# Kernel optimization log

Measured on AMD Instinct MI355X. Metric: run time of the kernel, lower is better.

## Reference

```python
import jax, jax.numpy as jnp
import numpy as np

B, S, D_MODEL, N_HEADS = 4, 2048, 1024, 16
HEAD_DIM = D_MODEL // N_HEADS


def setup_inputs() -> dict:
    key = jax.random.key(0)
    k_x, k_wqkv, k_bqkv, k_wout, k_bout = jax.random.split(key, 5)
    x = jax.random.normal(k_x, (B, S, D_MODEL), dtype=jnp.float32)
    # causal mask: True = masked (matches masked_fill semantics)
    mask = jnp.triu(jnp.ones((S, S), dtype=bool), k=1)[None, None, :, :]
    sc = 1.0 / np.sqrt(D_MODEL)
    w_qkv = jax.random.normal(k_wqkv, (3 * D_MODEL, D_MODEL), dtype=jnp.float32) * sc
    b_qkv = jax.random.normal(k_bqkv, (3 * D_MODEL,), dtype=jnp.float32) * 0.02
    w_out = jax.random.normal(k_wout, (D_MODEL, D_MODEL), dtype=jnp.float32) * sc
    b_out = jax.random.normal(k_bout, (D_MODEL,), dtype=jnp.float32) * 0.02
    return {"x": x, "mask": mask, "w_qkv": w_qkv, "b_qkv": b_qkv,
            "w_out": w_out, "b_out": b_out}


def reference(x, mask, w_qkv, b_qkv, w_out, b_out):
    b, s, d = x.shape
    qkv = x @ w_qkv.T + b_qkv                      # [B,S,3*D]
    qkv = qkv.reshape(b, s, 3, N_HEADS, HEAD_DIM)
    q = qkv[:, :, 0].transpose(0, 2, 1, 3)         # [B,H,S,Dh]
    k = qkv[:, :, 1].transpose(0, 2, 1, 3)
    v = qkv[:, :, 2].transpose(0, 2, 1, 3)
    scores = jnp.einsum('bhqd,bhkd->bhqk', q, k) / np.sqrt(HEAD_DIM)
    scores = jnp.where(mask, -jnp.inf, scores)
    attn = jax.nn.softmax(scores, axis=-1)         # dropout p=0.0 -> identity
    ctx = jnp.einsum('bhqk,bhkd->bhqd', attn, v)   # [B,H,S,Dh]
    ctx = ctx.transpose(0, 2, 1, 3).reshape(b, s, d)
    return ctx @ w_out.T + b_out
```

## Files before the change

kernel.cpp:

```cpp
#include <hip/hip_runtime.h>
#include <stdint.h>

typedef __attribute__((ext_vector_type(8))) short bf16x8;
typedef __attribute__((ext_vector_type(4))) float f32x4;
typedef unsigned short u16;

#define NUM_B 4
#define SEQ   2048
#define DM    1024
#define NH    16
#define DH    64
#define M_TOT (NUM_B * SEQ)

__device__ __forceinline__ float bf2f(u16 u) {
    union { unsigned int i; float f; } c; c.i = ((unsigned int)u) << 16; return c.f;
}
__device__ __forceinline__ u16 f2bf(float f) {
    union { float f; unsigned int i; } c; c.f = f;
    unsigned int u = c.i;
    return (u16)((u + 0x7FFFu + ((u >> 16) & 1u)) >> 16);
}
__device__ __forceinline__ unsigned int pack2(float a, float b) {
    return (unsigned int)f2bf(a) | ((unsigned int)f2bf(b) << 16);
}

__device__ __forceinline__ u16 f2bf_hw(float a) {
    unsigned int r;
    asm("v_cvt_pk_bf16_f32 %0, %1, %2" : "=v"(r) : "v"(a), "v"(0.0f));
    return (u16)r;
}

#if __has_builtin(__builtin_amdgcn_exp2f)
#define EXP2F __builtin_amdgcn_exp2f
#else
#define EXP2F exp2f
#endif

#define GLOAD_LDS16(g, l)                                                     \
    __builtin_amdgcn_global_load_lds(                                         \
        (const __attribute__((address_space(1))) void*)(g),                   \
        (__attribute__((address_space(3))) void*)(l), 16, 0, 0)

__global__ void detect_dtype(const u16* __restrict__ x, int* __restrict__ flag) {
    __shared__ int cnt;
    if (threadIdx.x == 0) cnt = 0;
    __syncthreads();
    int local = 0;
    for (int i = threadIdx.x; i < 4096; i += 256) {
        const u16 v = x[i];
        const int e = (v >> 7) & 0xFF;
        if (v == 0 || (e >= 110 && e <= 145)) local++;
    }
    atomicAdd(&cnt, local);
    __syncthreads();
    if (threadIdx.x == 0) *flag = (cnt >= 3686) ? 0 : 1;
}

__global__ void convert_bf16(const void* __restrict__ in, u16* __restrict__ out,
                             long n, const int* __restrict__ flag)
{
    const long i0 = ((long)blockIdx.x * 256 + threadIdx.x) * 8;
    const long stride = (long)gridDim.x * 256 * 8;
    if (*flag) {
        const float* f = (const float*)in;
        for (long i = i0; i < n; i += stride) {
            float4 a = *(const float4*)(f + i);
            float4 b = *(const float4*)(f + i + 4);
            uint4 o;
            o.x = pack2(a.x, a.y); o.y = pack2(a.z, a.w);
            o.z = pack2(b.x, b.y); o.w = pack2(b.z, b.w);
            *(uint4*)(out + i) = o;
        }
    } else {
        const uint4* s = (const uint4*)in;
        for (long i = i0; i < n; i += stride)
            *(uint4*)(out + i) = s[i >> 3];
    }
}

template <int MODE, int N_TOT>
__global__ __launch_bounds__(256) void gemm_bt(
    const u16* __restrict__ A, const u16* __restrict__ Bm,
    const u16* __restrict__ bias,
    void* __restrict__ out0v, u16* __restrict__ out1, u16* __restrict__ out2,
    const int* __restrict__ outf32, long out_off)
{
    __shared__ __align__(16) u16 As[128 * 32];
    __shared__ __align__(16) u16 Bs[128 * 32];
    const int K = 1024;

    const int tid  = threadIdx.x;
    const int wave = tid >> 6;
    const int lane = tid & 63;
    const int l15  = lane & 15;
    const int quad = lane >> 4;

    const int m0 = blockIdx.y * 128;
    const int n0 = blockIdx.x * 128;
    const int wm = (wave >> 1) * 64;
    const int wn = (wave & 1) * 64;

    const int srow = lane >> 2;
    const int soff = (lane & 3) * 8;

    f32x4 acc[4][4];
#pragma unroll
    for (int i = 0; i < 4; ++i)
#pragma unroll
        for (int j = 0; j < 4; ++j)
            acc[i][j] = (f32x4){0.f, 0.f, 0.f, 0.f};

    for (int k0 = 0; k0 < K; k0 += 32) {
#pragma unroll
        for (int r = 0; r < 2; ++r) {
            const int chunk = wave * 2 + r;
            const int row   = chunk * 16 + srow;
            GLOAD_LDS16(&A[(size_t)(m0 + row) * K + k0 + soff], &As[chunk * 512]);
            GLOAD_LDS16(&Bm[(size_t)(n0 + row) * K + k0 + soff], &Bs[chunk * 512]);
        }
        __syncthreads();

        bf16x8 af[4], bfv[4];
#pragma unroll
        for (int i = 0; i < 4; ++i)
            af[i] = *(const bf16x8*)(&As[(wm + i * 16 + l15) * 32 + quad * 8]);
#pragma unroll
        for (int j = 0; j < 4; ++j)
            bfv[j] = *(const bf16x8*)(&Bs[(wn + j * 16 + l15) * 32 + quad * 8]);

#pragma unroll
        for (int i = 0; i < 4; ++i)
#pragma unroll
            for (int j = 0; j < 4; ++j)
                acc[i][j] = __builtin_amdgcn_mfma_f32_16x16x32_bf16(
                    af[i], bfv[j], acc[i][j], 0, 0, 0);
        __syncthreads();
    }

    const int of32 = outf32 ? *outf32 : 0;
#pragma unroll
    for (int j = 0; j < 4; ++j) {
        const int n  = n0 + wn + j * 16 + l15;
        const float bv = bf2f(bias[n]);
#pragma unroll
        for (int i = 0; i < 4; ++i) {
#pragma unroll
            for (int reg = 0; reg < 4; ++reg) {
                const int m = m0 + wm + i * 16 + quad * 4 + reg;
                const float v = acc[i][j][reg] + bv;
                if (MODE == 0) {
                    const int sel = n >> 10;
                    const int h   = (n >> 6) & 15;
                    const int dh  = n & 63;
                    const int b   = m >> 11;
                    const int s   = m & 2047;
                    if (sel == 2) {
                        out2[((size_t)((b * NH + h) * DH + dh)) * SEQ + s] = f2bf(v);
                    } else {
                        u16* dst = (sel == 0) ? (u16*)out0v : out1;
                        dst[((size_t)((b * NH + h) * SEQ + s)) * DH + dh] = f2bf(v);
                    }
                } else {
                    if (of32)
                        ((float*)out0v)[out_off + (size_t)m * N_TOT + n] = v;
                    else
                        ((u16*)out0v)[out_off + (size_t)m * N_TOT + n] = f2bf(v);
                }
            }
        }
    }
}

__global__ __launch_bounds__(256) void attn_fwd(
    const u16* __restrict__ Qb, const u16* __restrict__ Kb,
    const u16* __restrict__ Vt, u16* __restrict__ ctx)
{
    __shared__ __align__(16) u16 Ks[2][2048];
    __shared__ __align__(16) u16 Vs[2][2048];
    __shared__ __align__(16) short Pbuf[4][2][16 * 40];

    const int tid  = threadIdx.x;
    const int wave = tid >> 6;
    const int lane = tid & 63;
    const int l15  = lane & 15;
    const int quad = lane >> 4;

    const int bh = blockIdx.x;
    const int yb = blockIdx.y;
    const int qrowA = (wave < 2) ? (yb * 64 + wave * 32)
                                 : (1984 - yb * 64 + (wave - 2) * 32);
    const int mkt   = qrowA >> 5;
    const int ktend = 63 - 2 * yb;

    const size_t base  = (size_t)bh * SEQ * DH;
    const size_t baseT = (size_t)bh * DH * SEQ;
    const float sc_l2e = 0.18033688011112042f;

    bf16x8 qf[2][2];
#pragma unroll
    for (int f = 0; f < 2; ++f)
#pragma unroll
        for (int c = 0; c < 2; ++c)
            qf[f][c] = *(const bf16x8*)(&Qb[base + (size_t)(qrowA + f * 16 + l15) * DH + c * 32 + quad * 8]);

    f32x4 acc[2][4];
#pragma unroll
    for (int f = 0; f < 2; ++f)
#pragma unroll
        for (int j = 0; j < 4; ++j) acc[f][j] = (f32x4){0.f, 0.f, 0.f, 0.f};
    float lsum[2][4] = {{0.f, 0.f, 0.f, 0.f}, {0.f, 0.f, 0.f, 0.f}};

    const int k_r = (wave & 1) * 16 + l15;
    const int k_c = ((wave >> 1) * 4 + quad) * 8;
    const int v_dh = wave * 16 + l15;
    const int v_k  = quad * 8;

    {
        GLOAD_LDS16(&Kb[base + (size_t)k_r * DH + k_c], &Ks[0][wave * 512]);
        GLOAD_LDS16(&Vt[baseT + (size_t)v_dh * SEQ + v_k], &Vs[0][wave * 512]);
    }

    for (int kt = 0; kt <= ktend; ++kt) {
        const int cur = kt & 1;
        __syncthreads();

        if (kt + 1 <= ktend) {
            const int nk0 = (kt + 1) * 32;
            GLOAD_LDS16(&Kb[base + (size_t)(nk0 + k_r) * DH + k_c],
                        &Ks[1 - cur][wave * 512]);
            GLOAD_LDS16(&Vt[baseT + (size_t)v_dh * SEQ + nk0 + v_k],
                        &Vs[1 - cur][wave * 512]);
        }

        if (kt <= mkt) {
            bf16x8 kf[2][2], vfr[4];
#pragma unroll
            for (int half = 0; half < 2; ++half)
#pragma unroll
                for (int c = 0; c < 2; ++c)
                    kf[half][c] = *(const bf16x8*)(&Ks[cur][(c * 2 + half) * 512 + lane * 8]);
#pragma unroll
            for (int j = 0; j < 4; ++j)
                vfr[j] = *(const bf16x8*)(&Vs[cur][j * 512 + lane * 8]);

            const int diag = (kt == mkt);
#pragma unroll
            for (int f = 0; f < 2; ++f) {
                f32x4 sc0 = (f32x4){0.f, 0.f, 0.f, 0.f};
                f32x4 sc1 = (f32x4){0.f, 0.f, 0.f, 0.f};
                sc0 = __builtin_amdgcn_mfma_f32_16x16x32_bf16(qf[f][0], kf[0][0], sc0, 0, 0, 0);
                sc0 = __builtin_amdgcn_mfma_f32_16x16x32_bf16(qf[f][1], kf[0][1], sc0, 0, 0, 0);
                sc1 = __builtin_amdgcn_mfma_f32_16x16x32_bf16(qf[f][0], kf[1][0], sc1, 0, 0, 0);
                sc1 = __builtin_amdgcn_mfma_f32_16x16x32_bf16(qf[f][1], kf[1][1], sc1, 0, 0, 0);

                float pa[4], pb[4];
                if (diag) {
#pragma unroll
                    for (int r = 0; r < 4; ++r) {
                        const int rr = quad * 4 + r;
                        if (f == 0) {
                            pa[r] = (l15 <= rr) ? EXP2F(sc0[r] * sc_l2e) : 0.f;
                            pb[r] = 0.f;
                        } else {
                            pa[r] = EXP2F(sc0[r] * sc_l2e);
                            pb[r] = (l15 <= rr) ? EXP2F(sc1[r] * sc_l2e) : 0.f;
                        }
                    }
                } else {
#pragma unroll
                    for (int r = 0; r < 4; ++r) {
                        pa[r] = EXP2F(sc0[r] * sc_l2e);
                        pb[r] = EXP2F(sc1[r] * sc_l2e);
                    }
                }
#pragma unroll
                for (int r = 0; r < 4; ++r)
                    lsum[f][r] += pa[r] + pb[r];

                short* pw = Pbuf[wave][f];
                asm volatile("" ::: "memory");
#pragma unroll
                for (int r = 0; r < 4; ++r) {
                    const int row = quad * 4 + r;
                    pw[row * 40 + l15]      = (short)f2bf_hw(pa[r]);
                    pw[row * 40 + 16 + l15] = (short)f2bf_hw(pb[r]);
                }
                asm volatile("" ::: "memory");
                const bf16x8 pf = *(const bf16x8*)(&pw[l15 * 40 + quad * 8]);

#pragma unroll
                for (int j = 0; j < 4; ++j)
                    acc[f][j] = __builtin_amdgcn_mfma_f32_16x16x32_bf16(pf, vfr[j], acc[f][j], 0, 0, 0);
            }
        }
    }

#pragma unroll
    for (int off = 1; off <= 8; off <<= 1)
#pragma unroll
        for (int f = 0; f < 2; ++f)
#pragma unroll
            for (int r = 0; r < 4; ++r)
                lsum[f][r] += __shfl_xor(lsum[f][r], off);

    const int b = bh >> 4;
    const int h = bh & 15;
#pragma unroll
    for (int f = 0; f < 2; ++f) {
#pragma unroll
        for (int r = 0; r < 4; ++r) {
            const float invL = 1.0f / lsum[f][r];
            const int qrow = qrowA + f * 16 + quad * 4 + r;
            const size_t rowaddr = ((size_t)(b * SEQ + qrow)) * DM + h * DH;
#pragma unroll
            for (int j = 0; j < 4; ++j)
                ctx[rowaddr + j * 16 + l15] = f2bf_hw(acc[f][j][r] * invL);
        }
    }
}

extern "C" void kernel_launch(void* const* d_in, const int* in_sizes, int n_in,
                              void* d_out, int out_size, void* d_ws, size_t ws_size,
                              hipStream_t stream)
{
    auto find = [&](long want, int fb) -> const void* {
        for (int i = 0; i < n_in; ++i)
            if ((long)in_sizes[i] == want) return d_in[i];
        if (fb >= n_in) fb = n_in - 1;
        return d_in[fb];
    };
    const void* x     = find(8388608, 0);
    const void* w_qkv = find(3145728, 2);
    const void* b_qkv = find(3072,    3);
    const void* w_out = find(1048576, 4);
    const void* b_out = find(1024,    5);

    char* ws   = (char*)d_ws;
    int*  flag = (int*)ws;
    char* p    = ws + 256;

    u16* xbf    = (u16*)p;                 p += (size_t)8388608 * 2;
    u16* wqkvbf = (u16*)p;                 p += (size_t)3145728 * 2;
    u16* bqkvbf = (u16*)p;                 p += 8192;
    u16* woutbf = (u16*)p;                 p += (size_t)1048576 * 2;
    u16* boutbf = (u16*)p;                 p += 8192;

    const size_t tensor_bytes = (size_t)M_TOT * DM * sizeof(u16);
    const size_t chunk_bytes  = tensor_bytes / NUM_B;
    const size_t conv_end     = (size_t)(p - ws);

    detect_dtype<<<1, 256, 0, stream>>>((const u16*)x, flag);
    auto cgrid = [](long n) { long g = (n / 8 + 255) / 256; return (int)(g > 2048 ? 2048 : g); };
    convert_bf16<<<cgrid(8388608), 256, 0, stream>>>(x,     xbf,    8388608, flag);
    convert_bf16<<<cgrid(3145728), 256, 0, stream>>>(w_qkv, wqkvbf, 3145728, flag);
    convert_bf16<<<cgrid(3072),    256, 0, stream>>>(b_qkv, bqkvbf, 3072,    flag);
    convert_bf16<<<cgrid(1048576), 256, 0, stream>>>(w_out, woutbf, 1048576, flag);
    convert_bf16<<<cgrid(1024),    256, 0, stream>>>(b_out, boutbf, 1024,    flag);

    if (ws_size >= conv_end + 4 * tensor_bytes) {
        u16* Qb  = (u16*)(ws + conv_end);
        u16* Kb  = (u16*)(ws + conv_end + tensor_bytes);
        u16* Vb  = (u16*)(ws + conv_end + 2 * tensor_bytes);
        u16* ctx = (u16*)(ws + conv_end + 3 * tensor_bytes);

        gemm_bt<0, 3072><<<dim3(24, 64), 256, 0, stream>>>(
            xbf, wqkvbf, bqkvbf, Qb, Kb, Vb, nullptr, 0);
        attn_fwd<<<dim3(NUM_B * NH, SEQ / 128), 256, 0, stream>>>(Qb, Kb, Vb, ctx);
        gemm_bt<1, 1024><<<dim3(8, 64), 256, 0, stream>>>(
            ctx, woutbf, boutbf, d_out, nullptr, nullptr, flag, 0);
    } else {
        u16* Qb  = (u16*)(ws + conv_end);
        u16* Kb  = (u16*)(ws + conv_end + chunk_bytes);
        u16* Vb  = (u16*)(ws + conv_end + 2 * chunk_bytes);
        u16* ctx = (u16*)(ws + conv_end + 3 * chunk_bytes);
        for (int b = 0; b < NUM_B; ++b) {
            const long eoff = (long)b * SEQ * DM;
            gemm_bt<0, 3072><<<dim3(24, 16), 256, 0, stream>>>(
                xbf + eoff, wqkvbf, bqkvbf, Qb, Kb, Vb, nullptr, 0);
            attn_fwd<<<dim3(NH, SEQ / 128), 256, 0, stream>>>(Qb, Kb, Vb, ctx);
            gemm_bt<1, 1024><<<dim3(8, 16), 256, 0, stream>>>(
                ctx, woutbf, boutbf, d_out, nullptr, nullptr, flag, eoff);
        }
    }
}
```

Measured before the change: 351.5 us.

## Load K/V fragments directly from global memory, drop LDS staging and block syncs

New measurement: 366.0 us. 4.1% more time.

```diff
diff --git a/kernel.cpp b/kernel.cpp
--- a/kernel.cpp
+++ b/kernel.cpp
@@ -175,8 +175,6 @@
     const u16* __restrict__ Qb, const u16* __restrict__ Kb,
     const u16* __restrict__ Vt, u16* __restrict__ ctx)
 {
-    __shared__ __align__(16) u16 Ks[2][2048];
-    __shared__ __align__(16) u16 Vs[2][2048];
     __shared__ __align__(16) short Pbuf[4][2][16 * 40];
 
     const int tid  = threadIdx.x;
@@ -190,7 +188,6 @@
     const int qrowA = (wave < 2) ? (yb * 64 + wave * 32)
                                  : (1984 - yb * 64 + (wave - 2) * 32);
     const int mkt   = qrowA >> 5;
-    const int ktend = 63 - 2 * yb;
 
     const size_t base  = (size_t)bh * SEQ * DH;
     const size_t baseT = (size_t)bh * DH * SEQ;
@@ -210,88 +207,69 @@
         for (int j = 0; j < 4; ++j) acc[f][j] = (f32x4){0.f, 0.f, 0.f, 0.f};
     float lsum[2][4] = {{0.f, 0.f, 0.f, 0.f}, {0.f, 0.f, 0.f, 0.f}};
 
-    const int k_r = (wave & 1) * 16 + l15;
-    const int k_c = ((wave >> 1) * 4 + quad) * 8;
-    const int v_dh = wave * 16 + l15;
-    const int v_k  = quad * 8;
-
-    {
-        GLOAD_LDS16(&Kb[base + (size_t)k_r * DH + k_c], &Ks[0][wave * 512]);
-        GLOAD_LDS16(&Vt[baseT + (size_t)v_dh * SEQ + v_k], &Vs[0][wave * 512]);
-    }
-
-    for (int kt = 0; kt <= ktend; ++kt) {
-        const int cur = kt & 1;
-        __syncthreads();
-
-        if (kt + 1 <= ktend) {
-            const int nk0 = (kt + 1) * 32;
-            GLOAD_LDS16(&Kb[base + (size_t)(nk0 + k_r) * DH + k_c],
-                        &Ks[1 - cur][wave * 512]);
-            GLOAD_LDS16(&Vt[baseT + (size_t)v_dh * SEQ + nk0 + v_k],
-                        &Vs[1 - cur][wave * 512]);
-        }
-
-        if (kt <= mkt) {
-            bf16x8 kf[2][2], vfr[4];
-#pragma unroll
-            for (int half = 0; half < 2; ++half)
-#pragma unroll
-                for (int c = 0; c < 2; ++c)
-                    kf[half][c] = *(const bf16x8*)(&Ks[cur][(c * 2 + half) * 512 + lane * 8]);
-#pragma unroll
-            for (int j = 0; j < 4; ++j)
-                vfr[j] = *(const bf16x8*)(&Vs[cur][j * 512 + lane * 8]);
-
-            const int diag = (kt == mkt);
-#pragma unroll
-            for (int f = 0; f < 2; ++f) {
-                f32x4 sc0 = (f32x4){0.f, 0.f, 0.f, 0.f};
-                f32x4 sc1 = (f32x4){0.f, 0.f, 0.f, 0.f};
-                sc0 = __builtin_amdgcn_mfma_f32_16x16x32_bf16(qf[f][0], kf[0][0], sc0, 0, 0, 0);
-                sc0 = __builtin_amdgcn_mfma_f32_16x16x32_bf16(qf[f][1], kf[0][1], sc0, 0, 0, 0);
-                sc1 = __builtin_amdgcn_mfma_f32_16x16x32_bf16(qf[f][0], kf[1][0], sc1, 0, 0, 0);
-                sc1 = __builtin_amdgcn_mfma_f32_16x16x32_bf16(qf[f][1], kf[1][1], sc1, 0, 0, 0);
-
-                float pa[4], pb[4];
-                if (diag) {
-#pragma unroll
-                    for (int r = 0; r < 4; ++r) {
-                        const int rr = quad * 4 + r;
-                        if (f == 0) {
-                            pa[r] = (l15 <= rr) ? EXP2F(sc0[r] * sc_l2e) : 0.f;
-                            pb[r] = 0.f;
-                        } else {
-                            pa[r] = EXP2F(sc0[r] * sc_l2e);
-                            pb[r] = (l15 <= rr) ? EXP2F(sc1[r] * sc_l2e) : 0.f;
-                        }
-                    }
-                } else {
-#pragma unroll
-                    for (int r = 0; r < 4; ++r) {
+    for (int kt = 0; kt <= mkt; ++kt) {
+        const int k0 = kt * 32;
+
+        bf16x8 kf[2][2], vfr[4];
+#pragma unroll
+        for (int half = 0; half < 2; ++half)
+#pragma unroll
+            for (int c = 0; c < 2; ++c)
+                kf[half][c] = *(const bf16x8*)(
+                    &Kb[base + (size_t)(k0 + half * 16 + l15) * DH + c * 32 + quad * 8]);
+#pragma unroll
+        for (int j = 0; j < 4; ++j)
+            vfr[j] = *(const bf16x8*)(
+                &Vt[baseT + (size_t)(j * 16 + l15) * SEQ + k0 + quad * 8]);
+
+        const int diag = (kt == mkt);
+#pragma unroll
+        for (int f = 0; f < 2; ++f) {
+            f32x4 sc0 = (f32x4){0.f, 0.f, 0.f, 0.f};
+            f32x4 sc1 = (f32x4){0.f, 0.f, 0.f, 0.f};
+            sc0 = __builtin_amdgcn_mfma_f32_16x16x32_bf16(qf[f][0], kf[0][0], sc0, 0, 0, 0);
+            sc0 = __builtin_amdgcn_mfma_f32_16x16x32_bf16(qf[f][1], kf[0][1], sc0, 0, 0, 0);
+            sc1 = __builtin_amdgcn_mfma_f32_16x16x32_bf16(qf[f][0], kf[1][0], sc1, 0, 0, 0);
+            sc1 = __builtin_amdgcn_mfma_f32_16x16x32_bf16(qf[f][1], kf[1][1], sc1, 0, 0, 0);
+
+            float pa[4], pb[4];
+            if (diag) {
+#pragma unroll
+                for (int r = 0; r < 4; ++r) {
+                    const int rr = quad * 4 + r;
+                    if (f == 0) {
+                        pa[r] = (l15 <= rr) ? EXP2F(sc0[r] * sc_l2e) : 0.f;
+                        pb[r] = 0.f;
+                    } else {
                         pa[r] = EXP2F(sc0[r] * sc_l2e);
-                        pb[r] = EXP2F(sc1[r] * sc_l2e);
+                        pb[r] = (l15 <= rr) ? EXP2F(sc1[r] * sc_l2e) : 0.f;
                     }
                 }
-#pragma unroll
-                for (int r = 0; r < 4; ++r)
-                    lsum[f][r] += pa[r] + pb[r];
-
-                short* pw = Pbuf[wave][f];
-                asm volatile("" ::: "memory");
+            } else {
 #pragma unroll
                 for (int r = 0; r < 4; ++r) {
-                    const int row = quad * 4 + r;
-                    pw[row * 40 + l15]      = (short)f2bf_hw(pa[r]);
-                    pw[row * 40 + 16 + l15] = (short)f2bf_hw(pb[r]);
+                    pa[r] = EXP2F(sc0[r] * sc_l2e);
+                    pb[r] = EXP2F(sc1[r] * sc_l2e);
                 }
-                asm volatile("" ::: "memory");
-                const bf16x8 pf = *(const bf16x8*)(&pw[l15 * 40 + quad * 8]);
-
-#pragma unroll
-                for (int j = 0; j < 4; ++j)
-                    acc[f][j] = __builtin_amdgcn_mfma_f32_16x16x32_bf16(pf, vfr[j], acc[f][j], 0, 0, 0);
             }
+#pragma unroll
+            for (int r = 0; r < 4; ++r)
+                lsum[f][r] += pa[r] + pb[r];
+
+            short* pw = Pbuf[wave][f];
+            asm volatile("" ::: "memory");
+#pragma unroll
+            for (int r = 0; r < 4; ++r) {
+                const int row = quad * 4 + r;
+                pw[row * 40 + l15]      = (short)f2bf_hw(pa[r]);
+                pw[row * 40 + 16 + l15] = (short)f2bf_hw(pb[r]);
+            }
+            asm volatile("" ::: "memory");
+            const bf16x8 pf = *(const bf16x8*)(&pw[l15 * 40 + quad * 8]);
+
+#pragma unroll
+            for (int j = 0; j < 4; ++j)
+                acc[f][j] = __builtin_amdgcn_mfma_f32_16x16x32_bf16(pf, vfr[j], acc[f][j], 0, 0, 0);
         }
     }
 
```
